# Optimization experiments

Hardware: AMD Instinct MI355X
Metric: run time of the kernel (lower is better)

## Reference

```python
import jax, jax.numpy as jnp
import numpy as np

NUM_NODES = 100000
NUM_EDGES = 1600000
IN_DIM = 64
OUT_DIM = 64


def setup_inputs() -> dict:
    key = jax.random.key(0)
    ks = jax.random.split(key, 8)
    x = jax.random.normal(ks[0], (NUM_NODES, IN_DIM), dtype=jnp.float32)
    edge_index = jax.random.randint(ks[1], (2, NUM_EDGES), 0, NUM_NODES, dtype=jnp.int64)
    s = 1.0 / np.sqrt(2 * IN_DIM)
    w1 = jax.random.uniform(ks[2], (2 * IN_DIM, OUT_DIM), jnp.float32, -s, s)
    b1 = jax.random.uniform(ks[3], (OUT_DIM,), jnp.float32, -s, s)
    s2 = 1.0 / np.sqrt(OUT_DIM)
    w2 = jax.random.uniform(ks[4], (OUT_DIM, OUT_DIM), jnp.float32, -s2, s2)
    b2 = jax.random.uniform(ks[5], (OUT_DIM,), jnp.float32, -s2, s2)
    s3 = 1.0 / np.sqrt(IN_DIM)
    ws = jax.random.uniform(ks[6], (IN_DIM, OUT_DIM), jnp.float32, -s3, s3)
    bs = jax.random.uniform(ks[7], (OUT_DIM,), jnp.float32, -s3, s3)
    return {"x": x, "edge_index": edge_index, "w1": w1, "b1": b1,
            "w2": w2, "b2": b2, "ws": ws, "bs": bs}


def reference(x, edge_index, w1, b1, w2, b2, ws, bs):
    num_nodes = x.shape[0]
    src, dst = edge_index[0], edge_index[1]
    # self term: (N, out)
    h_self = x @ ws + bs
    # gather endpoints and run 2-layer MLP on concatenated features: (E, out)
    msg = jnp.concatenate([x[src], x[dst]], axis=-1)
    msg = jax.nn.relu(msg @ w1 + b1)
    msg = msg @ w2 + b2
    # mean aggregation over dst
    agg = jax.ops.segment_sum(msg, dst, num_segments=num_nodes)
    deg = jax.ops.segment_sum(jnp.ones_like(dst, dtype=x.dtype), dst,
                              num_segments=num_nodes)
    deg = jnp.clip(deg, 1.0, None)
    out = agg / deg[:, None] + h_self
    return out
```

## Files before the change

kernel.cpp:

```cpp
#include <hip/hip_runtime.h>
#include <hip/hip_bf16.h>

#define NN 100000
#define EE 1600000
#define NB 1563
#define NSUB 8
#define CAPS 240
#define NBC 98
#define CAPC 17408
#define CHA 2048
#define NBLA 782
#define NLIN ((NN + 63) / 64)

#define OFF_CNT 0u
#define OFF_DEG 50432u
#define OFF_BUF 450560u
#define OFF_P   12454400u
#define OFF_Q   25254400u
#define OFF_U   38054400u

__device__ __forceinline__ ushort f2bf(float f) {
  unsigned u = __float_as_uint(f);
  unsigned r = (u + 0x7FFFu + ((u >> 16) & 1u)) >> 16;
  return (ushort)r;
}
__device__ __forceinline__ float bf2f(ushort h) {
  return __uint_as_float(((unsigned)h) << 16);
}
__device__ __forceinline__ unsigned pk2(float a, float b) {
  return (unsigned)f2bf(a) | ((unsigned)f2bf(b) << 16);
}

__launch_bounds__(256)
__global__ void k_binA(const int* __restrict__ ei, int* __restrict__ ccnt,
                       unsigned* __restrict__ cbuf) {
  __shared__ int hist[NBC], offs[NBC], starts[NBC], gbase[NBC];
  __shared__ int wtot[4];
  __shared__ unsigned sorted[CHA];
  __shared__ ushort bkt[CHA];
  int t = threadIdx.x;
  if (t < NBC) hist[t] = 0;
  __syncthreads();
  unsigned ent[8];
  int cb[8];
  int e0 = blockIdx.x * CHA;
  #pragma unroll
  for (int it = 0; it < 8; ++it) {
    int e = e0 + t + it * 256;
    cb[it] = -1;
    if (e < EE) {
      int s = ei[e], d = ei[EE + e];
      ent[it] = (unsigned)s | ((unsigned)(d & 1023) << 17);
      cb[it] = d >> 10;
      atomicAdd(&hist[cb[it]], 1);
    }
  }
  __syncthreads();
  {
    int v = (t < NBC) ? hist[t] : 0;
    int x = v;
    #pragma unroll
    for (int off = 1; off < 64; off <<= 1) {
      int w = __shfl_up(x, off);
      if ((t & 63) >= off) x += w;
    }
    if ((t & 63) == 63) wtot[t >> 6] = x;
    __syncthreads();
    int pre = 0;
    #pragma unroll
    for (int w = 0; w < 4; ++w)
      if (w < (t >> 6)) pre += wtot[w];
    if (t < NBC) { offs[t] = pre + x - v; starts[t] = pre + x - v; }
  }
  __syncthreads();
  #pragma unroll
  for (int it = 0; it < 8; ++it) {
    if (cb[it] >= 0) {
      int pos = atomicAdd(&offs[cb[it]], 1);
      sorted[pos] = ent[it];
      bkt[pos] = (ushort)cb[it];
    }
  }
  __syncthreads();
  if (t < NBC) {
    int c = hist[t];
    gbase[t] = (c > 0) ? atomicAdd(&ccnt[t], c) : 0;
  }
  __syncthreads();
  int tot = min(EE - e0, CHA);
  for (int i = t; i < tot; i += 256) {
    int b = bkt[i];
    int dst = gbase[b] + (i - starts[b]);
    if (dst < CAPC) cbuf[b * CAPC + dst] = sorted[i];
  }
}

__launch_bounds__(256)
__global__ void k_binB(const int* __restrict__ ccnt, const unsigned* __restrict__ cbuf,
                       int* __restrict__ cnt, unsigned* __restrict__ buf) {
  __shared__ int hist[16], offs[16], starts[16], gbase[16];
  __shared__ unsigned sorted[2304];
  int t = threadIdx.x;
  int cb = blockIdx.x >> 3;
  int j  = blockIdx.x & 7;
  if (t < 16) hist[t] = 0;
  __syncthreads();
  int tot = min(ccnt[cb], CAPC);
  int beg = (tot * j) >> 3;
  int end = (tot * (j + 1)) >> 3;
  int n = end - beg;
  unsigned ent[9];
  int fb[9];
  #pragma unroll
  for (int it = 0; it < 9; ++it) {
    int i = t + it * 256;
    fb[it] = -1;
    if (i < n) {
      unsigned e = cbuf[cb * CAPC + beg + i];
      ent[it] = e;
      fb[it] = (int)(e >> 23);
      atomicAdd(&hist[fb[it]], 1);
    }
  }
  __syncthreads();
  if (t < 16) {
    int v = hist[t], x = v;
    #pragma unroll
    for (int off = 1; off < 16; off <<= 1) {
      int w = __shfl_up(x, off);
      if (t >= off) x += w;
    }
    offs[t] = x - v;
    starts[t] = x - v;
  }
  __syncthreads();
  #pragma unroll
  for (int it = 0; it < 9; ++it) {
    if (fb[it] >= 0) {
      int pos = atomicAdd(&offs[fb[it]], 1);
      sorted[pos] = ent[it];
    }
  }
  __syncthreads();
  if (t < 16) {
    int c = hist[t];
    int fbg = cb * 16 + t;
    gbase[t] = (c > 0 && fbg < NB) ? atomicAdd(&cnt[j * NB + fbg], c) : 0;
  }
  __syncthreads();
  for (int i = t; i < n; i += 256) {
    unsigned e = sorted[i];
    int b = (int)(e >> 23);
    int fbg = cb * 16 + b;
    int dst = gbase[b] + (i - starts[b]);
    if (dst < CAPS && fbg < NB)
      buf[(unsigned)(j * NB + fbg) * CAPS + dst] = e & 0x7FFFFFu;
  }
}

__launch_bounds__(256)
__global__ void k_lin1(const float* __restrict__ x, const float* __restrict__ w1,
                       const float* __restrict__ b1, ushort* __restrict__ P,
                       ushort* __restrict__ Qb) {
  __shared__ float w1s[128 * 64];
  __shared__ float xs[64 * 66];
  int t = threadIdx.x;
  int base = blockIdx.x * 64;
  #pragma unroll
  for (int i = 0; i < 8; ++i) {
    int idx4 = t + i * 256;
    reinterpret_cast<float4*>(w1s)[idx4] = reinterpret_cast<const float4*>(w1)[idx4];
  }
  #pragma unroll
  for (int i = 0; i < 4; ++i) {
    int idx4 = t + i * 256;
    int r = idx4 >> 4, c = idx4 & 15;
    int grow = base + r;
    float4 v = make_float4(0.f, 0.f, 0.f, 0.f);
    if (grow < NN) v = reinterpret_cast<const float4*>(x)[grow * 16 + c];
    float* p = &xs[r * 66 + c * 4];
    *reinterpret_cast<float2*>(p) = make_float2(v.x, v.y);
    *reinterpret_cast<float2*>(p + 2) = make_float2(v.z, v.w);
  }
  __syncthreads();
  int tr = t >> 4, tc = t & 15;
  int half = tc >> 3;
  int c0 = (tc & 7) * 8;
  float acc[4][8];
  #pragma unroll
  for (int i = 0; i < 4; ++i)
    #pragma unroll
    for (int j = 0; j < 8; ++j) acc[i][j] = 0.f;
  #pragma unroll 4
  for (int k = 0; k < 64; ++k) {
    float a0 = xs[(4 * tr + 0) * 66 + k];
    float a1 = xs[(4 * tr + 1) * 66 + k];
    float a2 = xs[(4 * tr + 2) * 66 + k];
    float a3 = xs[(4 * tr + 3) * 66 + k];
    const float* bp = &w1s[(half * 64 + k) * 64 + c0];
    float4 w0 = *reinterpret_cast<const float4*>(bp);
    float4 w1v = *reinterpret_cast<const float4*>(bp + 4);
    float wf[8] = {w0.x, w0.y, w0.z, w0.w, w1v.x, w1v.y, w1v.z, w1v.w};
    #pragma unroll
    for (int j = 0; j < 8; ++j) {
      acc[0][j] = fmaf(a0, wf[j], acc[0][j]);
      acc[1][j] = fmaf(a1, wf[j], acc[1][j]);
      acc[2][j] = fmaf(a2, wf[j], acc[2][j]);
      acc[3][j] = fmaf(a3, wf[j], acc[3][j]);
    }
  }
  if (half) {
    #pragma unroll
    for (int j = 0; j < 8; ++j) {
      float bv = b1[c0 + j];
      #pragma unroll
      for (int i = 0; i < 4; ++i) acc[i][j] += bv;
    }
  }
  ushort* dstb = (half ? Qb : P);
  #pragma unroll
  for (int i = 0; i < 4; ++i) {
    int row = base + 4 * tr + i;
    if (row < NN) {
      uint4 o = make_uint4(pk2(acc[i][0], acc[i][1]), pk2(acc[i][2], acc[i][3]),
                           pk2(acc[i][4], acc[i][5]), pk2(acc[i][6], acc[i][7]));
      *reinterpret_cast<uint4*>(&dstb[row * 64 + c0]) = o;
    }
  }
}

__launch_bounds__(256)
__global__ void k_agg(const int* __restrict__ cnt, const unsigned* __restrict__ buf,
                      const uint2* __restrict__ P2, const uint2* __restrict__ Q2,
                      ushort* __restrict__ U, int* __restrict__ deg) {
  __shared__ unsigned sorted[NSUB * CAPS];
  __shared__ int hist[64], offs[64], starts[64];
  int b = blockIdx.x;
  int t = threadIdx.x;
  if (t < 64) hist[t] = 0;
  __syncthreads();
  int cs[NSUB];
  #pragma unroll
  for (int s = 0; s < NSUB; ++s) {
    cs[s] = min(cnt[s * NB + b], CAPS);
    for (int i = t; i < cs[s]; i += 256)
      atomicAdd(&hist[buf[(s * NB + b) * CAPS + i] >> 17], 1);
  }
  __syncthreads();
  if (t < 64) {
    int v = hist[t], ex = v;
    #pragma unroll
    for (int off = 1; off < 64; off <<= 1) {
      int w = __shfl_up(ex, off);
      if ((t & 63) >= off) ex += w;
    }
    offs[t] = ex - v;
    starts[t] = ex - v;
  }
  __syncthreads();
  #pragma unroll
  for (int s = 0; s < NSUB; ++s) {
    for (int i = t; i < cs[s]; i += 256) {
      unsigned e = buf[(s * NB + b) * CAPS + i];
      int pos = atomicAdd(&offs[e >> 17], 1);
      sorted[pos] = e & 0x1FFFFu;
    }
  }
  __syncthreads();
  int lane = t & 63;
  int w = t >> 6;
  int eg = lane >> 4;
  int c = lane & 15;
  for (int k = 0; k < 16; ++k) {
    int nl = w * 16 + k;
    int n = b * 64 + nl;
    if (n >= NN) break;
    int dg = hist[nl];
    int st = starts[nl];
    uint2 q = Q2[n * 16 + c];
    float q0 = bf2f((ushort)(q.x & 0xFFFFu)), q1 = bf2f((ushort)(q.x >> 16));
    float q2 = bf2f((ushort)(q.y & 0xFFFFu)), q3 = bf2f((ushort)(q.y >> 16));
    float a0 = 0.f, a1 = 0.f, a2 = 0.f, a3 = 0.f;
    int e = st + eg, eend = st + dg;
    while (e + 4 < eend) {
      unsigned s0 = sorted[e];
      unsigned s1 = sorted[e + 4];
      uint2 p0 = P2[s0 * 16 + c];
      uint2 p1 = P2[s1 * 16 + c];
      a0 += fmaxf(bf2f((ushort)(p0.x & 0xFFFFu)) + q0, 0.f);
      a1 += fmaxf(bf2f((ushort)(p0.x >> 16)) + q1, 0.f);
      a2 += fmaxf(bf2f((ushort)(p0.y & 0xFFFFu)) + q2, 0.f);
      a3 += fmaxf(bf2f((ushort)(p0.y >> 16)) + q3, 0.f);
      a0 += fmaxf(bf2f((ushort)(p1.x & 0xFFFFu)) + q0, 0.f);
      a1 += fmaxf(bf2f((ushort)(p1.x >> 16)) + q1, 0.f);
      a2 += fmaxf(bf2f((ushort)(p1.y & 0xFFFFu)) + q2, 0.f);
      a3 += fmaxf(bf2f((ushort)(p1.y >> 16)) + q3, 0.f);
      e += 8;
    }
    if (e < eend) {
      unsigned s0 = sorted[e];
      uint2 p0 = P2[s0 * 16 + c];
      a0 += fmaxf(bf2f((ushort)(p0.x & 0xFFFFu)) + q0, 0.f);
      a1 += fmaxf(bf2f((ushort)(p0.x >> 16)) + q1, 0.f);
      a2 += fmaxf(bf2f((ushort)(p0.y & 0xFFFFu)) + q2, 0.f);
      a3 += fmaxf(bf2f((ushort)(p0.y >> 16)) + q3, 0.f);
    }
    a0 += __shfl_xor(a0, 16); a0 += __shfl_xor(a0, 32);
    a1 += __shfl_xor(a1, 16); a1 += __shfl_xor(a1, 32);
    a2 += __shfl_xor(a2, 16); a2 += __shfl_xor(a2, 32);
    a3 += __shfl_xor(a3, 16); a3 += __shfl_xor(a3, 32);
    if (eg == 0) {
      float inv = 1.f / (float)max(dg, 1);
      reinterpret_cast<uint2*>(U)[n * 16 + c] =
          make_uint2(pk2(a0 * inv, a1 * inv), pk2(a2 * inv, a3 * inv));
    }
  }
  if (t < 64 && b * 64 + t < NN) deg[b * 64 + t] = hist[t];
}

__launch_bounds__(256)
__global__ void k_final(const float* __restrict__ x, const ushort* __restrict__ U,
                        const float* __restrict__ w2, const float* __restrict__ b2,
                        const float* __restrict__ wsw, const float* __restrict__ bs,
                        const int* __restrict__ deg, float* __restrict__ out) {
  __shared__ float Wss[128 * 64];
  __shared__ float ts[64 * 66];
  int t = threadIdx.x;
  int base = blockIdx.x * 64;
  #pragma unroll
  for (int i = 0; i < 4; ++i) {
    int idx4 = t + i * 256;
    reinterpret_cast<float4*>(Wss)[idx4] = reinterpret_cast<const float4*>(w2)[idx4];
    reinterpret_cast<float4*>(Wss)[idx4 + 1024] = reinterpret_cast<const float4*>(wsw)[idx4];
  }
  #pragma unroll
  for (int i = 0; i < 4; ++i) {
    int idx = t + i * 256;
    int r = idx >> 4, c = idx & 15;
    int grow = base + r;
    uint2 v = make_uint2(0u, 0u);
    if (grow < NN) v = reinterpret_cast<const uint2*>(U)[grow * 16 + c];
    float* p = &ts[r * 66 + c * 4];
    p[0] = bf2f((ushort)(v.x & 0xFFFFu));
    p[1] = bf2f((ushort)(v.x >> 16));
    p[2] = bf2f((ushort)(v.y & 0xFFFFu));
    p[3] = bf2f((ushort)(v.y >> 16));
  }
  __syncthreads();
  int tr = t >> 4, tc = t & 15;
  float acc[4][4];
  #pragma unroll
  for (int i = 0; i < 4; ++i)
    #pragma unroll
    for (int j = 0; j < 4; ++j) acc[i][j] = 0.f;
  #pragma unroll 4
  for (int k = 0; k < 64; ++k) {
    float a0 = ts[(4 * tr + 0) * 66 + k];
    float a1 = ts[(4 * tr + 1) * 66 + k];
    float a2 = ts[(4 * tr + 2) * 66 + k];
    float a3 = ts[(4 * tr + 3) * 66 + k];
    float4 wv = *reinterpret_cast<const float4*>(&Wss[k * 64 + 4 * tc]);
    acc[0][0] = fmaf(a0, wv.x, acc[0][0]); acc[0][1] = fmaf(a0, wv.y, acc[0][1]);
    acc[0][2] = fmaf(a0, wv.z, acc[0][2]); acc[0][3] = fmaf(a0, wv.w, acc[0][3]);
    acc[1][0] = fmaf(a1, wv.x, acc[1][0]); acc[1][1] = fmaf(a1, wv.y, acc[1][1]);
    acc[1][2] = fmaf(a1, wv.z, acc[1][2]); acc[1][3] = fmaf(a1, wv.w, acc[1][3]);
    acc[2][0] = fmaf(a2, wv.x, acc[2][0]); acc[2][1] = fmaf(a2, wv.y, acc[2][1]);
    acc[2][2] = fmaf(a2, wv.z, acc[2][2]); acc[2][3] = fmaf(a2, wv.w, acc[2][3]);
    acc[3][0] = fmaf(a3, wv.x, acc[3][0]); acc[3][1] = fmaf(a3, wv.y, acc[3][1]);
    acc[3][2] = fmaf(a3, wv.z, acc[3][2]); acc[3][3] = fmaf(a3, wv.w, acc[3][3]);
  }
  __syncthreads();
  #pragma unroll
  for (int i = 0; i < 4; ++i) {
    int idx4 = t + i * 256;
    int r = idx4 >> 4, cc = idx4 & 15;
    int grow = base + r;
    float4 v = make_float4(0.f, 0.f, 0.f, 0.f);
    if (grow < NN) v = reinterpret_cast<const float4*>(x)[grow * 16 + cc];
    float* p = &ts[r * 66 + cc * 4];
    *reinterpret_cast<float2*>(p) = make_float2(v.x, v.y);
    *reinterpret_cast<float2*>(p + 2) = make_float2(v.z, v.w);
  }
  __syncthreads();
  #pragma unroll 4
  for (int k = 0; k < 64; ++k) {
    float a0 = ts[(4 * tr + 0) * 66 + k];
    float a1 = ts[(4 * tr + 1) * 66 + k];
    float a2 = ts[(4 * tr + 2) * 66 + k];
    float a3 = ts[(4 * tr + 3) * 66 + k];
    float4 wv = *reinterpret_cast<const float4*>(&Wss[(64 + k) * 64 + 4 * tc]);
    acc[0][0] = fmaf(a0, wv.x, acc[0][0]); acc[0][1] = fmaf(a0, wv.y, acc[0][1]);
    acc[0][2] = fmaf(a0, wv.z, acc[0][2]); acc[0][3] = fmaf(a0, wv.w, acc[0][3]);
    acc[1][0] = fmaf(a1, wv.x, acc[1][0]); acc[1][1] = fmaf(a1, wv.y, acc[1][1]);
    acc[1][2] = fmaf(a1, wv.z, acc[1][2]); acc[1][3] = fmaf(a1, wv.w, acc[1][3]);
    acc[2][0] = fmaf(a2, wv.x, acc[2][0]); acc[2][1] = fmaf(a2, wv.y, acc[2][1]);
    acc[2][2] = fmaf(a2, wv.z, acc[2][2]); acc[2][3] = fmaf(a2, wv.w, acc[2][3]);
    acc[3][0] = fmaf(a3, wv.x, acc[3][0]); acc[3][1] = fmaf(a3, wv.y, acc[3][1]);
    acc[3][2] = fmaf(a3, wv.z, acc[3][2]); acc[3][3] = fmaf(a3, wv.w, acc[3][3]);
  }
  #pragma unroll
  for (int i = 0; i < 4; ++i) {
    int rl = 4 * tr + i;
    int row = base + rl;
    if (row < NN) {
      float bsc = (deg[row] > 0) ? 1.f : 0.f;
      float4 o;
      o.x = acc[i][0] + bs[4 * tc + 0] + bsc * b2[4 * tc + 0];
      o.y = acc[i][1] + bs[4 * tc + 1] + bsc * b2[4 * tc + 1];
      o.z = acc[i][2] + bs[4 * tc + 2] + bsc * b2[4 * tc + 2];
      o.w = acc[i][3] + bs[4 * tc + 3] + bsc * b2[4 * tc + 3];
      *reinterpret_cast<float4*>(&out[row * 64 + 4 * tc]) = o;
    }
  }
}

extern "C" void kernel_launch(void* const* d_in, const int* in_sizes, int n_in,
                              void* d_out, int out_size, void* d_ws, size_t ws_size,
                              hipStream_t stream) {
  const float* x   = (const float*)d_in[0];
  const int*   ei  = (const int*)d_in[1];
  const float* w1  = (const float*)d_in[2];
  const float* b1  = (const float*)d_in[3];
  const float* w2  = (const float*)d_in[4];
  const float* b2  = (const float*)d_in[5];
  const float* wsw = (const float*)d_in[6];
  const float* bs  = (const float*)d_in[7];
  float* out = (float*)d_out;
  char* ws = (char*)d_ws;
  int* cnt       = (int*)(ws + OFF_CNT);
  int* ccnt      = cnt + NSUB * NB;
  int* deg       = (int*)(ws + OFF_DEG);
  unsigned* buf  = (unsigned*)(ws + OFF_BUF);
  ushort* P      = (ushort*)(ws + OFF_P);
  ushort* Qb     = (ushort*)(ws + OFF_Q);
  ushort* U      = (ushort*)(ws + OFF_U);
  unsigned* cbuf = (unsigned*)(ws + OFF_U);

  hipMemsetAsync(cnt, 0, (NSUB * NB + NBC) * sizeof(int), stream);
  k_binA<<<NBLA, 256, 0, stream>>>(ei, ccnt, cbuf);
  k_binB<<<NBC * 8, 256, 0, stream>>>(ccnt, cbuf, cnt, buf);
  k_lin1<<<NLIN, 256, 0, stream>>>(x, w1, b1, P, Qb);
  k_agg<<<NB, 256, 0, stream>>>(cnt, buf, (const uint2*)P, (const uint2*)Qb, U, deg);
  k_final<<<NLIN, 256, 0, stream>>>(x, U, w2, b2, wsw, bs, deg, out);
}
```

Measured before the change: 229.9 us.

## Replace two-level binning with per-coarse-bucket CSR build and feature-split aggregation

```diff
diff --git a/kernel.cpp b/kernel.cpp
--- a/kernel.cpp
+++ b/kernel.cpp
@@ -3,21 +3,21 @@
 
 #define NN 100000
 #define EE 1600000
-#define NB 1563
-#define NSUB 8
-#define CAPS 240
 #define NBC 98
 #define CAPC 17408
 #define CHA 2048
 #define NBLA 782
 #define NLIN ((NN + 63) / 64)
-
-#define OFF_CNT 0u
-#define OFF_DEG 50432u
-#define OFF_BUF 450560u
-#define OFF_P   12454400u
-#define OFF_Q   25254400u
-#define OFF_U   38054400u
+#define NTILE 3125
+#define NAGG (NTILE * 8)
+
+#define OFF_CCNT 0u
+#define OFF_DEG  512u
+#define OFF_NS   400640u
+#define OFF_CBUF 800768u
+#define OFF_CSR  7624704u
+#define OFF_P    14448640u
+#define OFF_Q    27248640u
 
 __device__ __forceinline__ ushort f2bf(float f) {
   unsigned u = __float_as_uint(f);
@@ -29,6 +29,12 @@
 }
 __device__ __forceinline__ unsigned pk2(float a, float b) {
   return (unsigned)f2bf(a) | ((unsigned)f2bf(b) << 16);
+}
+__device__ __forceinline__ float uplo(unsigned u) {
+  return __uint_as_float(u << 16);
+}
+__device__ __forceinline__ float uphi(unsigned u) {
+  return __uint_as_float(u & 0xFFFF0000u);
 }
 
 __launch_bounds__(256)
@@ -95,66 +101,57 @@
   }
 }
 
-__launch_bounds__(256)
-__global__ void k_binB(const int* __restrict__ ccnt, const unsigned* __restrict__ cbuf,
-                       int* __restrict__ cnt, unsigned* __restrict__ buf) {
-  __shared__ int hist[16], offs[16], starts[16], gbase[16];
-  __shared__ unsigned sorted[2304];
+__launch_bounds__(1024)
+__global__ void k_csr(const int* __restrict__ ccnt, const unsigned* __restrict__ cbuf,
+                      unsigned* __restrict__ csr, int* __restrict__ ns,
+                      int* __restrict__ deg) {
+  __shared__ int hist[1024], offs[1024], starts[1024], wpre[16];
+  int cb = blockIdx.x;
   int t = threadIdx.x;
-  int cb = blockIdx.x >> 3;
-  int j  = blockIdx.x & 7;
-  if (t < 16) hist[t] = 0;
+  hist[t] = 0;
   __syncthreads();
   int tot = min(ccnt[cb], CAPC);
-  int beg = (tot * j) >> 3;
-  int end = (tot * (j + 1)) >> 3;
-  int n = end - beg;
-  unsigned ent[9];
-  int fb[9];
-  #pragma unroll
-  for (int it = 0; it < 9; ++it) {
-    int i = t + it * 256;
-    fb[it] = -1;
-    if (i < n) {
-      unsigned e = cbuf[cb * CAPC + beg + i];
-      ent[it] = e;
-      fb[it] = (int)(e >> 23);
-      atomicAdd(&hist[fb[it]], 1);
-    }
-  }
-  __syncthreads();
-  if (t < 16) {
-    int v = hist[t], x = v;
-    #pragma unroll
-    for (int off = 1; off < 16; off <<= 1) {
-      int w = __shfl_up(x, off);
-      if (t >= off) x += w;
-    }
-    offs[t] = x - v;
-    starts[t] = x - v;
-  }
-  __syncthreads();
-  #pragma unroll
-  for (int it = 0; it < 9; ++it) {
-    if (fb[it] >= 0) {
-      int pos = atomicAdd(&offs[fb[it]], 1);
-      sorted[pos] = ent[it];
-    }
-  }
-  __syncthreads();
-  if (t < 16) {
-    int c = hist[t];
-    int fbg = cb * 16 + t;
-    gbase[t] = (c > 0 && fbg < NB) ? atomicAdd(&cnt[j * NB + fbg], c) : 0;
-  }
-  __syncthreads();
-  for (int i = t; i < n; i += 256) {
-    unsigned e = sorted[i];
-    int b = (int)(e >> 23);
-    int fbg = cb * 16 + b;
-    int dst = gbase[b] + (i - starts[b]);
-    if (dst < CAPS && fbg < NB)
-      buf[(unsigned)(j * NB + fbg) * CAPS + dst] = e & 0x7FFFFFu;
+  const unsigned* cb_base = cbuf + cb * CAPC;
+  for (int i = t; i < tot; i += 1024)
+    atomicAdd(&hist[cb_base[i] >> 17], 1);
+  __syncthreads();
+  {
+    int v = hist[t];
+    int x = v;
+    int lane = t & 63;
+    int w = t >> 6;
+    #pragma unroll
+    for (int off = 1; off < 64; off <<= 1) {
+      int q = __shfl_up(x, off);
+      if (lane >= off) x += q;
+    }
+    if (lane == 63) wpre[w] = x;
+    __syncthreads();
+    if (t < 16) {
+      int s = wpre[t];
+      int xx = s;
+      #pragma unroll
+      for (int off = 1; off < 16; off <<= 1) {
+        int q = __shfl_up(xx, off);
+        if (t >= off) xx += q;
+      }
+      wpre[t] = xx - s;
+    }
+    __syncthreads();
+    int ex = wpre[w] + x - v;
+    offs[t] = ex;
+    starts[t] = ex;
+  }
+  __syncthreads();
+  for (int i = t; i < tot; i += 1024) {
+    unsigned e = cb_base[i];
+    int pos = atomicAdd(&offs[e >> 17], 1);
+    csr[cb * CAPC + pos] = e & 0x1FFFFu;
+  }
+  int n = cb * 1024 + t;
+  if (n < NN) {
+    ns[n] = cb * CAPC + starts[t];
+    deg[n] = hist[t];
   }
 }
 
@@ -230,96 +227,62 @@
 }
 
 __launch_bounds__(256)
-__global__ void k_agg(const int* __restrict__ cnt, const unsigned* __restrict__ buf,
-                      const uint2* __restrict__ P2, const uint2* __restrict__ Q2,
-                      ushort* __restrict__ U, int* __restrict__ deg) {
-  __shared__ unsigned sorted[NSUB * CAPS];
-  __shared__ int hist[64], offs[64], starts[64];
-  int b = blockIdx.x;
+__global__ void k_agg(const unsigned* __restrict__ csr, const int* __restrict__ ns,
+                      const int* __restrict__ deg, const unsigned* __restrict__ Pu,
+                      const unsigned* __restrict__ Qu, float* __restrict__ U) {
   int t = threadIdx.x;
-  if (t < 64) hist[t] = 0;
-  __syncthreads();
-  int cs[NSUB];
-  #pragma unroll
-  for (int s = 0; s < NSUB; ++s) {
-    cs[s] = min(cnt[s * NB + b], CAPS);
-    for (int i = t; i < cs[s]; i += 256)
-      atomicAdd(&hist[buf[(s * NB + b) * CAPS + i] >> 17], 1);
-  }
-  __syncthreads();
-  if (t < 64) {
-    int v = hist[t], ex = v;
-    #pragma unroll
-    for (int off = 1; off < 64; off <<= 1) {
-      int w = __shfl_up(ex, off);
-      if ((t & 63) >= off) ex += w;
-    }
-    offs[t] = ex - v;
-    starts[t] = ex - v;
-  }
-  __syncthreads();
-  #pragma unroll
-  for (int s = 0; s < NSUB; ++s) {
-    for (int i = t; i < cs[s]; i += 256) {
-      unsigned e = buf[(s * NB + b) * CAPS + i];
-      int pos = atomicAdd(&offs[e >> 17], 1);
-      sorted[pos] = e & 0x1FFFFu;
-    }
-  }
-  __syncthreads();
+  int slot = blockIdx.x & 7;
+  int tile = blockIdx.x >> 3;
+  int f = slot >> 1;
+  int h = slot & 1;
+  int w = t >> 6;
   int lane = t & 63;
-  int w = t >> 6;
-  int eg = lane >> 4;
-  int c = lane & 15;
-  for (int k = 0; k < 16; ++k) {
-    int nl = w * 16 + k;
-    int n = b * 64 + nl;
-    if (n >= NN) break;
-    int dg = hist[nl];
-    int st = starts[nl];
-    uint2 q = Q2[n * 16 + c];
-    float q0 = bf2f((ushort)(q.x & 0xFFFFu)), q1 = bf2f((ushort)(q.x >> 16));
-    float q2 = bf2f((ushort)(q.y & 0xFFFFu)), q3 = bf2f((ushort)(q.y >> 16));
-    float a0 = 0.f, a1 = 0.f, a2 = 0.f, a3 = 0.f;
-    int e = st + eg, eend = st + dg;
-    while (e + 4 < eend) {
-      unsigned s0 = sorted[e];
-      unsigned s1 = sorted[e + 4];
-      uint2 p0 = P2[s0 * 16 + c];
-      uint2 p1 = P2[s1 * 16 + c];
-      a0 += fmaxf(bf2f((ushort)(p0.x & 0xFFFFu)) + q0, 0.f);
-      a1 += fmaxf(bf2f((ushort)(p0.x >> 16)) + q1, 0.f);
-      a2 += fmaxf(bf2f((ushort)(p0.y & 0xFFFFu)) + q2, 0.f);
-      a3 += fmaxf(bf2f((ushort)(p0.y >> 16)) + q3, 0.f);
-      a0 += fmaxf(bf2f((ushort)(p1.x & 0xFFFFu)) + q0, 0.f);
-      a1 += fmaxf(bf2f((ushort)(p1.x >> 16)) + q1, 0.f);
-      a2 += fmaxf(bf2f((ushort)(p1.y & 0xFFFFu)) + q2, 0.f);
-      a3 += fmaxf(bf2f((ushort)(p1.y >> 16)) + q3, 0.f);
+  int eg = lane >> 3;
+  int cu = lane & 7;
+  int fo = f * 8 + cu;
+  #pragma unroll
+  for (int g = 0; g < 4; ++g) {
+    int n = tile * 32 + h * 16 + w * 4 + g;
+    if (n >= NN) continue;
+    int dg = deg[n];
+    int st = ns[n];
+    unsigned q = Qu[n * 32 + fo];
+    float q0 = uplo(q), q1 = uphi(q);
+    float a0 = 0.f, a1 = 0.f;
+    int e = 0;
+    while (e + 16 <= dg) {
+      unsigned s0 = csr[st + e + eg];
+      unsigned s1 = csr[st + e + 8 + eg];
+      unsigned p0 = Pu[s0 * 32 + fo];
+      unsigned p1 = Pu[s1 * 32 + fo];
+      a0 += fmaxf(uplo(p0) + q0, 0.f); a1 += fmaxf(uphi(p0) + q1, 0.f);
+      a0 += fmaxf(uplo(p1) + q0, 0.f); a1 += fmaxf(uphi(p1) + q1, 0.f);
+      e += 16;
+    }
+    if (e + 8 <= dg) {
+      unsigned s0 = csr[st + e + eg];
+      unsigned p0 = Pu[s0 * 32 + fo];
+      a0 += fmaxf(uplo(p0) + q0, 0.f); a1 += fmaxf(uphi(p0) + q1, 0.f);
       e += 8;
     }
-    if (e < eend) {
-      unsigned s0 = sorted[e];
-      uint2 p0 = P2[s0 * 16 + c];
-      a0 += fmaxf(bf2f((ushort)(p0.x & 0xFFFFu)) + q0, 0.f);
-      a1 += fmaxf(bf2f((ushort)(p0.x >> 16)) + q1, 0.f);
-      a2 += fmaxf(bf2f((ushort)(p0.y & 0xFFFFu)) + q2, 0.f);
-      a3 += fmaxf(bf2f((ushort)(p0.y >> 16)) + q3, 0.f);
-    }
-    a0 += __shfl_xor(a0, 16); a0 += __shfl_xor(a0, 32);
-    a1 += __shfl_xor(a1, 16); a1 += __shfl_xor(a1, 32);
-    a2 += __shfl_xor(a2, 16); a2 += __shfl_xor(a2, 32);
-    a3 += __shfl_xor(a3, 16); a3 += __shfl_xor(a3, 32);
+    if (e + eg < dg) {
+      unsigned s0 = csr[st + e + eg];
+      unsigned p0 = Pu[s0 * 32 + fo];
+      a0 += fmaxf(uplo(p0) + q0, 0.f); a1 += fmaxf(uphi(p0) + q1, 0.f);
+    }
+    a0 += __shfl_xor(a0, 8);  a1 += __shfl_xor(a1, 8);
+    a0 += __shfl_xor(a0, 16); a1 += __shfl_xor(a1, 16);
+    a0 += __shfl_xor(a0, 32); a1 += __shfl_xor(a1, 32);
     if (eg == 0) {
       float inv = 1.f / (float)max(dg, 1);
-      reinterpret_cast<uint2*>(U)[n * 16 + c] =
-          make_uint2(pk2(a0 * inv, a1 * inv), pk2(a2 * inv, a3 * inv));
-    }
-  }
-  if (t < 64 && b * 64 + t < NN) deg[b * 64 + t] = hist[t];
+      *reinterpret_cast<float2*>(&U[n * 64 + f * 16 + cu * 2]) =
+          make_float2(a0 * inv, a1 * inv);
+    }
+  }
 }
 
 __launch_bounds__(256)
-__global__ void k_final(const float* __restrict__ x, const ushort* __restrict__ U,
+__global__ void k_final(const float* __restrict__ x, const float* __restrict__ U,
                         const float* __restrict__ w2, const float* __restrict__ b2,
                         const float* __restrict__ wsw, const float* __restrict__ bs,
                         const int* __restrict__ deg, float* __restrict__ out) {
@@ -335,16 +298,14 @@
   }
   #pragma unroll
   for (int i = 0; i < 4; ++i) {
-    int idx = t + i * 256;
-    int r = idx >> 4, c = idx & 15;
+    int idx4 = t + i * 256;
+    int r = idx4 >> 4, c = idx4 & 15;
     int grow = base + r;
-    uint2 v = make_uint2(0u, 0u);
-    if (grow < NN) v = reinterpret_cast<const uint2*>(U)[grow * 16 + c];
+    float4 v = make_float4(0.f, 0.f, 0.f, 0.f);
+    if (grow < NN) v = reinterpret_cast<const float4*>(U)[grow * 16 + c];
     float* p = &ts[r * 66 + c * 4];
-    p[0] = bf2f((ushort)(v.x & 0xFFFFu));
-    p[1] = bf2f((ushort)(v.x >> 16));
-    p[2] = bf2f((ushort)(v.y & 0xFFFFu));
-    p[3] = bf2f((ushort)(v.y >> 16));
+    *reinterpret_cast<float2*>(p) = make_float2(v.x, v.y);
+    *reinterpret_cast<float2*>(p + 2) = make_float2(v.z, v.w);
   }
   __syncthreads();
   int tr = t >> 4, tc = t & 15;
@@ -427,19 +388,19 @@
   const float* bs  = (const float*)d_in[7];
   float* out = (float*)d_out;
   char* ws = (char*)d_ws;
-  int* cnt       = (int*)(ws + OFF_CNT);
-  int* ccnt      = cnt + NSUB * NB;
+  int* ccnt      = (int*)(ws + OFF_CCNT);
   int* deg       = (int*)(ws + OFF_DEG);
-  unsigned* buf  = (unsigned*)(ws + OFF_BUF);
+  int* ns        = (int*)(ws + OFF_NS);
+  unsigned* cbuf = (unsigned*)(ws + OFF_CBUF);
+  unsigned* csr  = (unsigned*)(ws + OFF_CSR);
   ushort* P      = (ushort*)(ws + OFF_P);
   ushort* Qb     = (ushort*)(ws + OFF_Q);
-  ushort* U      = (ushort*)(ws + OFF_U);
-  unsigned* cbuf = (unsigned*)(ws + OFF_U);
-
-  hipMemsetAsync(cnt, 0, (NSUB * NB + NBC) * sizeof(int), stream);
+
+  hipMemsetAsync(ccnt, 0, NBC * sizeof(int), stream);
   k_binA<<<NBLA, 256, 0, stream>>>(ei, ccnt, cbuf);
-  k_binB<<<NBC * 8, 256, 0, stream>>>(ccnt, cbuf, cnt, buf);
   k_lin1<<<NLIN, 256, 0, stream>>>(x, w1, b1, P, Qb);
-  k_agg<<<NB, 256, 0, stream>>>(cnt, buf, (const uint2*)P, (const uint2*)Qb, U, deg);
-  k_final<<<NLIN, 256, 0, stream>>>(x, U, w2, b2, wsw, bs, deg, out);
-}
+  k_csr<<<NBC, 1024, 0, stream>>>(ccnt, cbuf, csr, ns, deg);
+  k_agg<<<NAGG, 256, 0, stream>>>(csr, ns, deg, (const unsigned*)P,
+                                  (const unsigned*)Qb, out);
+  k_final<<<NLIN, 256, 0, stream>>>(x, out, w2, b2, wsw, bs, deg, out);
+}
```

Result: slower. 307.4 us (+33.7%).
